# Optimization experiments

Measured on AMD Instinct MI355X. Metric: run time of the kernel, lower is better.

Reference implementation:

```python
import jax, jax.numpy as jnp
import numpy as np

NIBBLE_SHIFTS = jnp.arange(8, dtype=jnp.int32) * 4


def _unpack_int4(packed):
    # packed: [..., P] int32 -> [..., P*8] int32 values in [0, 15]
    vals = (packed[..., None] >> NIBBLE_SHIFTS) & 0xF
    return vals.reshape(*packed.shape[:-1], packed.shape[-1] * 8)


def setup_inputs() -> dict:
    key = jax.random.key(0)
    k1, k2, k3, k4, k5, k6 = jax.random.split(key, 6)
    M, K, N, G = 4096, 4096, 11008, 128
    inp = jax.random.normal(k1, (M, K), dtype=jnp.float32)
    qweight = jax.random.randint(k2, (K, N // 8), 0, 2147483647, dtype=jnp.int32)
    woq_scales = jax.random.uniform(k3, (K // G, N), dtype=jnp.float32)
    woq_qzeros = jax.random.randint(k4, (K // G, N // 8), 0, 2147483647, dtype=jnp.int32)
    woq_bias = jax.random.normal(k5, (N,), dtype=jnp.float32)
    mul = jax.random.normal(k6, (M, N), dtype=jnp.float32)
    return {"inp": inp, "qweight": qweight, "woq_scales": woq_scales,
            "woq_qzeros": woq_qzeros, "woq_bias": woq_bias, "mul": mul,
            "group_size": G}


def reference(inp, qweight, woq_scales, woq_qzeros, woq_bias, mul, group_size):
    K = qweight.shape[0]
    # dequantize int4 weights: w = (q - z) * scale, per group of `group_size` K-rows
    w_int = _unpack_int4(qweight).astype(jnp.float32)            # [K, N]
    z_int = _unpack_int4(woq_qzeros).astype(jnp.float32)         # [K/G, N]
    zeros_full = jnp.repeat(z_int, group_size, axis=0)           # [K, N]
    scales_full = jnp.repeat(woq_scales, group_size, axis=0)     # [K, N]
    w = (w_int - zeros_full) * scales_full                       # [K, N]
    woq_out = inp @ w + woq_bias                                 # [M, N]
    return jax.nn.silu(woq_out) * mul
```

## Files before the change

### kernel.cpp

```cpp
#include <hip/hip_runtime.h>
#include <hip/hip_bf16.h>

typedef __attribute__((ext_vector_type(8))) short short8;
typedef __attribute__((ext_vector_type(4))) short short4v;
typedef __attribute__((ext_vector_type(4))) float float4v;

__device__ __forceinline__ short f2bf(float f) {
  union { float f; unsigned u; } v; v.f = f;
  unsigned r = v.u + 0x7fffu + ((v.u >> 16) & 1u);
  return (short)(r >> 16);
}

typedef const __attribute__((address_space(1))) unsigned int* as1_u32p;
typedef __attribute__((address_space(3))) unsigned int* as3_u32p;

__device__ __forceinline__ void gl_lds16(const void* g, void* l) {
  __builtin_amdgcn_global_load_lds((as1_u32p)g, (as3_u32p)l, 16, 0, 0);
}

__global__ __launch_bounds__(256, 2)
void dequant_kernel(const int* __restrict__ qw,
                    const float* __restrict__ scales,
                    const int* __restrict__ qzeros,
                    short* __restrict__ Bt,
                    int K, int N, int G)
{
  __shared__ short Ls[128 * 64];
  const int N8  = N >> 3;
  const int k0  = blockIdx.x * 64;
  const int n80 = blockIdx.y * 16;
  const int g   = k0 / G;
  const int tid  = threadIdx.x;
  const int lane = tid & 63;
  const int w    = tid >> 6;

  const int4 q4 = *(const int4*)(qw + (size_t)(k0 + lane) * N8 + n80 + w * 4);
  const int4 z4 = *(const int4*)(qzeros + (size_t)g * N8 + n80 + w * 4);
  const int qa[4] = {q4.x, q4.y, q4.z, q4.w};
  const int za[4] = {z4.x, z4.y, z4.z, z4.w};

  #pragma unroll
  for (int it = 0; it < 4; ++it) {
    const int n8l = w * 4 + it;
    const float4v s0 = *(const float4v*)(scales + (size_t)g * N + (n80 + n8l) * 8);
    const float4v s1 = *(const float4v*)(scales + (size_t)g * N + (n80 + n8l) * 8 + 4);
    const float sc[8] = {s0[0], s0[1], s0[2], s0[3], s1[0], s1[1], s1[2], s1[3]};
    const int wq = qa[it], wz = za[it];
    #pragma unroll
    for (int j = 0; j < 8; ++j) {
      const float z = (float)((wz >> (4 * j)) & 0xF);
      const float q = (float)((wq >> (4 * j)) & 0xF);
      Ls[(n8l * 8 + j) * 64 + lane] = f2bf((q - z) * sc[j]);
    }
  }
  __syncthreads();

  #pragma unroll
  for (int it = 0; it < 4; ++it) {
    const int c   = tid + it * 256;
    const int row = c >> 3;
    const int off = (c & 7) * 8;
    const short8 v = *(const short8*)(&Ls[row * 64 + off]);
    *(short8*)(Bt + (size_t)(n80 * 8 + row) * K + k0 + off) = v;
  }
}

__global__ __launch_bounds__(256, 4)
void aconv_kernel(const float* __restrict__ in, short* __restrict__ out, long long n)
{
  const long long i = ((long long)blockIdx.x * blockDim.x + threadIdx.x) * 8;
  if (i >= n) return;
  const float4v a = *(const float4v*)(in + i);
  const float4v b = *(const float4v*)(in + i + 4);
  short8 h;
  h[0] = f2bf(a[0]); h[1] = f2bf(a[1]); h[2] = f2bf(a[2]); h[3] = f2bf(a[3]);
  h[4] = f2bf(b[0]); h[5] = f2bf(b[1]); h[6] = f2bf(b[2]); h[7] = f2bf(b[3]);
  *(short8*)(out + i) = h;
}

__global__ __launch_bounds__(512, 2)
void gemm256_silu_mul_kernel(const short* __restrict__ A,
                             const short* __restrict__ Bt,
                             const float* __restrict__ bias,
                             const float* __restrict__ mulp,
                             float*       __restrict__ out,
                             int M, int N, int K)
{
  __shared__ short L[2][2][16384];

  const int tid  = threadIdx.x;
  const int lane = tid & 63;
  const int wave = tid >> 6;
  const int wm   = wave >> 2;
  const int wn   = wave & 3;

  const int nwg = gridDim.x;
  const int q8 = nwg >> 3, r8 = nwg & 7;
  const int xcd = blockIdx.x & 7, sub = blockIdx.x >> 3;
  const int swz = (xcd < r8 ? xcd * (q8 + 1) : r8 * (q8 + 1) + (xcd - r8) * q8) + sub;
  const int nbx = N >> 8;
  const int bx = swz % nbx, by = swz / nbx;
  const int m0 = by << 8, n0 = bx << 8;

  const short* Ab = A  + (size_t)m0 * K;
  const short* Bb = Bt + (size_t)n0 * K;

  const int srow = lane >> 2;
  const int scol = (((lane & 3) ^ ((lane & 32) >> 4))) * 8;
  const int fm = lane & 15;
  const int ko = ((lane >> 4) * 8) ^ ((fm & 8) ? 16 : 0);

  const int BG0 = wave * 2;
  const int BG1 = wave * 2 + 1;
  const int AEg = (wave & 3) + (wave >> 2) * 8;
  const int ALg = AEg + 4;

  float4v acc[8][4];
  #pragma unroll
  for (int i = 0; i < 8; ++i)
    #pragma unroll
    for (int j = 0; j < 4; ++j)
      acc[i][j] = (float4v){0.f, 0.f, 0.f, 0.f};

  const int NT = K >> 6;

  auto stage2 = [&](int buf, int ab, int g, const short* __restrict__ base, int kk) {
    #pragma unroll
    for (int ks = 0; ks < 2; ++ks)
      gl_lds16(base + (size_t)(g * 16 + srow) * K + kk + ks * 32 + scol,
               &L[buf][ab][(g * 2 + ks) * 512]);
  };

  stage2(0, 1, BG0, Bb, 0);
  stage2(0, 1, BG1, Bb, 0);
  stage2(0, 0, AEg, Ab, 0);
  stage2(0, 0, ALg, Ab, 0);
  asm volatile("s_waitcnt vmcnt(2)" ::: "memory");
  __builtin_amdgcn_s_barrier();

  for (int t = 0; t < NT; ++t) {
    const int cur = t & 1;
    const int nxt = cur ^ 1;
    const int kk1 = (t + 1) << 6;
    const bool pf = (t + 1) < NT;

    short8 af[4][2], bf[4][2];

    #pragma unroll
    for (int i = 0; i < 4; ++i)
      #pragma unroll
      for (int ks = 0; ks < 2; ++ks)
        af[i][ks] = *(const short8*)(
            &L[cur][0][((wm * 8 + i) * 2 + ks) * 512 + fm * 32 + ko]);
    #pragma unroll
    for (int j = 0; j < 2; ++j)
      #pragma unroll
      for (int ks = 0; ks < 2; ++ks)
        bf[j][ks] = *(const short8*)(
            &L[cur][1][((wn * 4 + j) * 2 + ks) * 512 + fm * 32 + ko]);
    if (pf) stage2(nxt, 1, BG0, Bb, kk1);
    __builtin_amdgcn_s_barrier();
    asm volatile("s_waitcnt lgkmcnt(0)" ::: "memory");
    __builtin_amdgcn_sched_barrier(0);
    __builtin_amdgcn_s_setprio(1);
    #pragma unroll
    for (int i = 0; i < 4; ++i)
      #pragma unroll
      for (int j = 0; j < 2; ++j)
        #pragma unroll
        for (int ks = 0; ks < 2; ++ks)
          acc[i][j] = __builtin_amdgcn_mfma_f32_16x16x32_bf16(
              af[i][ks], bf[j][ks], acc[i][j], 0, 0, 0);
    __builtin_amdgcn_s_setprio(0);
    __builtin_amdgcn_s_barrier();

    #pragma unroll
    for (int j = 2; j < 4; ++j)
      #pragma unroll
      for (int ks = 0; ks < 2; ++ks)
        bf[j][ks] = *(const short8*)(
            &L[cur][1][((wn * 4 + j) * 2 + ks) * 512 + fm * 32 + ko]);
    if (pf) stage2(nxt, 1, BG1, Bb, kk1);
    __builtin_amdgcn_s_barrier();
    asm volatile("s_waitcnt lgkmcnt(0)" ::: "memory");
    __builtin_amdgcn_sched_barrier(0);
    __builtin_amdgcn_s_setprio(1);
    #pragma unroll
    for (int i = 0; i < 4; ++i)
      #pragma unroll
      for (int j = 2; j < 4; ++j)
        #pragma unroll
        for (int ks = 0; ks < 2; ++ks)
          acc[i][j] = __builtin_amdgcn_mfma_f32_16x16x32_bf16(
              af[i][ks], bf[j][ks], acc[i][j], 0, 0, 0);
    __builtin_amdgcn_s_setprio(0);
    if (pf) { asm volatile("s_waitcnt vmcnt(4)" ::: "memory"); }
    else    { asm volatile("s_waitcnt vmcnt(0)" ::: "memory"); }
    __builtin_amdgcn_s_barrier();

    #pragma unroll
    for (int i = 0; i < 4; ++i)
      #pragma unroll
      for (int ks = 0; ks < 2; ++ks)
        af[i][ks] = *(const short8*)(
            &L[cur][0][((wm * 8 + 4 + i) * 2 + ks) * 512 + fm * 32 + ko]);
    if (pf) stage2(nxt, 0, AEg, Ab, kk1);
    __builtin_amdgcn_s_barrier();
    asm volatile("s_waitcnt lgkmcnt(0)" ::: "memory");
    __builtin_amdgcn_sched_barrier(0);
    __builtin_amdgcn_s_setprio(1);
    #pragma unroll
    for (int i = 0; i < 4; ++i)
      #pragma unroll
      for (int j = 0; j < 2; ++j)
        #pragma unroll
        for (int ks = 0; ks < 2; ++ks)
          acc[4 + i][j] = __builtin_amdgcn_mfma_f32_16x16x32_bf16(
              af[i][ks], bf[j][ks], acc[4 + i][j], 0, 0, 0);
    __builtin_amdgcn_s_setprio(0);
    __builtin_amdgcn_s_barrier();

    if (pf) stage2(nxt, 0, ALg, Ab, kk1);
    __builtin_amdgcn_s_barrier();
    __builtin_amdgcn_s_setprio(1);
    #pragma unroll
    for (int i = 0; i < 4; ++i)
      #pragma unroll
      for (int j = 2; j < 4; ++j)
        #pragma unroll
        for (int ks = 0; ks < 2; ++ks)
          acc[4 + i][j] = __builtin_amdgcn_mfma_f32_16x16x32_bf16(
              af[i][ks], bf[j][ks], acc[4 + i][j], 0, 0, 0);
    __builtin_amdgcn_s_setprio(0);
    if (pf) { asm volatile("s_waitcnt vmcnt(2)" ::: "memory"); }
    __builtin_amdgcn_s_barrier();
  }

  const int cn  = lane & 15;
  const int cr4 = (lane >> 4) * 4;
  #pragma unroll
  for (int mt = 0; mt < 8; ++mt) {
    #pragma unroll
    for (int nt = 0; nt < 4; ++nt) {
      const int n  = n0 + wn * 64 + nt * 16 + cn;
      const float bn = bias[n];
      #pragma unroll
      for (int i = 0; i < 4; ++i) {
        const int m = m0 + wm * 128 + mt * 16 + cr4 + i;
        float x = acc[mt][nt][i] + bn;
        float s = x / (1.0f + __expf(-x));
        out[(size_t)m * N + n] = s * mulp[(size_t)m * N + n];
      }
    }
  }
}

__global__ __launch_bounds__(256, 2)
void gemm_silu_mul_kernel(const short* __restrict__ A,
                          const short* __restrict__ Bt,
                          const float* __restrict__ bias,
                          const float* __restrict__ mulp,
                          float*       __restrict__ out,
                          int M, int N, int K)
{
  __shared__ short As[128 * 64];
  __shared__ short Bs[128 * 64];

  const int tid  = threadIdx.x;
  const int lane = tid & 63;
  const int wave = tid >> 6;
  const int wr = (wave >> 1) * 64;
  const int wc = (wave & 1) * 64;
  const int m0 = blockIdx.y * 128;
  const int n0 = blockIdx.x * 128;

  float4v acc[4][4];
  #pragma unroll
  for (int i = 0; i < 4; ++i)
    #pragma unroll
    for (int j = 0; j < 4; ++j)
      acc[i][j] = (float4v){0.f, 0.f, 0.f, 0.f};

  const int fm = lane & 15;
  const int fk = (lane >> 4) * 8;
  const int srow = lane >> 3;
  const int scol = (lane & 7) * 8;

  for (int k0 = 0; k0 < K; k0 += 64) {
    #pragma unroll
    for (int c = 0; c < 4; ++c) {
      const int chunk = wave * 4 + c;
      const int row   = chunk * 8 + srow;
      gl_lds16(A  + (size_t)(m0 + row) * K + k0 + scol, &As[chunk * 512]);
      gl_lds16(Bt + (size_t)(n0 + row) * K + k0 + scol, &Bs[chunk * 512]);
    }
    __syncthreads();

    #pragma unroll
    for (int ks = 0; ks < 64; ks += 32) {
      short8 a[4], b[4];
      #pragma unroll
      for (int mt = 0; mt < 4; ++mt)
        a[mt] = *(const short8*)(&As[(wr + mt * 16 + fm) * 64 + ks + fk]);
      #pragma unroll
      for (int nt = 0; nt < 4; ++nt)
        b[nt] = *(const short8*)(&Bs[(wc + nt * 16 + fm) * 64 + ks + fk]);
      #pragma unroll
      for (int mt = 0; mt < 4; ++mt)
        #pragma unroll
        for (int nt = 0; nt < 4; ++nt)
          acc[mt][nt] = __builtin_amdgcn_mfma_f32_16x16x32_bf16(a[mt], b[nt], acc[mt][nt], 0, 0, 0);
    }
    __syncthreads();
  }

  const int cn = lane & 15;
  const int cr = (lane >> 4) * 4;
  #pragma unroll
  for (int mt = 0; mt < 4; ++mt) {
    #pragma unroll
    for (int nt = 0; nt < 4; ++nt) {
      const int n  = n0 + wc + nt * 16 + cn;
      const float bn = bias[n];
      #pragma unroll
      for (int i = 0; i < 4; ++i) {
        const int m = m0 + wr + mt * 16 + cr + i;
        float x = acc[mt][nt][i] + bn;
        float s = x / (1.0f + __expf(-x));
        out[(size_t)m * N + n] = s * mulp[(size_t)m * N + n];
      }
    }
  }
}

#define BM 128
#define BN 128
#define BK 64
#define LDA 72
#define LDB 72

__global__ __launch_bounds__(256, 2)
void woq_silu_mul_kernel(const float* __restrict__ inp, const int* __restrict__ qw,
                         const float* __restrict__ scales, const int* __restrict__ qzeros,
                         const float* __restrict__ bias, const float* __restrict__ mulp,
                         float* __restrict__ out, int M, int N, int K, int G)
{
  __shared__ short As[BM * LDA];
  __shared__ short Bs[BN * LDB];
  const int tid  = threadIdx.x;
  const int lane = tid & 63;
  const int wave = tid >> 6;
  const int wr = (wave >> 1) * 64;
  const int wc = (wave & 1) * 64;
  const int m0 = blockIdx.y * BM;
  const int n0 = blockIdx.x * BN;
  const int N8 = N >> 3;
  float4v acc[4][4];
  #pragma unroll
  for (int i = 0; i < 4; ++i)
    #pragma unroll
    for (int j = 0; j < 4; ++j)
      acc[i][j] = (float4v){0.f, 0.f, 0.f, 0.f};
  const int n8l  = tid >> 4;
  const int kloc = (tid & 15) * 4;
  const int fm = lane & 15;
  const int fk = (lane >> 4) * 8;
  for (int k0 = 0; k0 < K; k0 += BK) {
    #pragma unroll
    for (int i = 0; i < 8; ++i) {
      int f = tid + i * 256;
      int row = f >> 4;
      int col = (f & 15) * 4;
      float4v a4 = *(const float4v*)(inp + (size_t)(m0 + row) * K + k0 + col);
      short4v h;
      h[0] = f2bf(a4[0]); h[1] = f2bf(a4[1]); h[2] = f2bf(a4[2]); h[3] = f2bf(a4[3]);
      *(short4v*)(&As[row * LDA + col]) = h;
    }
    {
      const int g = k0 / G;
      const int n8g = (n0 >> 3) + n8l;
      const int zw = qzeros[(size_t)g * N8 + n8g];
      const float4v s0 = *(const float4v*)(scales + (size_t)g * N + n0 + n8l * 8);
      const float4v s1 = *(const float4v*)(scales + (size_t)g * N + n0 + n8l * 8 + 4);
      float sc[8] = {s0[0], s0[1], s0[2], s0[3], s1[0], s1[1], s1[2], s1[3]};
      int w[4];
      #pragma unroll
      for (int kk = 0; kk < 4; ++kk)
        w[kk] = qw[(size_t)(k0 + kloc + kk) * N8 + n8g];
      #pragma unroll
      for (int j = 0; j < 8; ++j) {
        const float zj = (float)((zw >> (4 * j)) & 0xF);
        const float sj = sc[j];
        short4v h;
        #pragma unroll
        for (int kk = 0; kk < 4; ++kk) {
          int q = (w[kk] >> (4 * j)) & 0xF;
          h[kk] = f2bf(((float)q - zj) * sj);
        }
        *(short4v*)(&Bs[(n8l * 8 + j) * LDB + kloc]) = h;
      }
    }
    __syncthreads();
    #pragma unroll
    for (int ks = 0; ks < BK; ks += 32) {
      short8 a[4], b[4];
      #pragma unroll
      for (int mt = 0; mt < 4; ++mt)
        a[mt] = *(const short8*)(&As[(wr + mt * 16 + fm) * LDA + ks + fk]);
      #pragma unroll
      for (int nt = 0; nt < 4; ++nt)
        b[nt] = *(const short8*)(&Bs[(wc + nt * 16 + fm) * LDB + ks + fk]);
      #pragma unroll
      for (int mt = 0; mt < 4; ++mt)
        #pragma unroll
        for (int nt = 0; nt < 4; ++nt)
          acc[mt][nt] = __builtin_amdgcn_mfma_f32_16x16x32_bf16(a[mt], b[nt], acc[mt][nt], 0, 0, 0);
    }
    __syncthreads();
  }
  const int cn = lane & 15;
  const int cr = (lane >> 4) * 4;
  #pragma unroll
  for (int mt = 0; mt < 4; ++mt) {
    #pragma unroll
    for (int nt = 0; nt < 4; ++nt) {
      const int n = n0 + wc + nt * 16 + cn;
      const float bn = bias[n];
      #pragma unroll
      for (int i = 0; i < 4; ++i) {
        const int m = m0 + wr + mt * 16 + cr + i;
        float x = acc[mt][nt][i] + bn;
        float s = x / (1.0f + __expf(-x));
        out[(size_t)m * N + n] = s * mulp[(size_t)m * N + n];
      }
    }
  }
}

extern "C" void kernel_launch(void* const* d_in, const int* in_sizes, int n_in,
                              void* d_out, int out_size, void* d_ws, size_t ws_size,
                              hipStream_t stream) {
  const float* inp    = (const float*)d_in[0];
  const int*   qw     = (const int*)d_in[1];
  const float* scales = (const float*)d_in[2];
  const int*   qzeros = (const int*)d_in[3];
  const float* bias   = (const float*)d_in[4];
  const float* mulp   = (const float*)d_in[5];
  float*       out    = (float*)d_out;

  const int N = in_sizes[4];
  const int K = (int)(((long long)in_sizes[1] * 8) / N);
  const int M = (int)((long long)in_sizes[0] / K);
  const int G = K / (in_sizes[2] / N);

  const size_t btBytes = (size_t)N * K * sizeof(short);
  const size_t aBytes  = (size_t)M * K * sizeof(short);

  if (ws_size >= btBytes + aBytes) {
    short* Bt  = (short*)d_ws;
    short* Abf = (short*)((char*)d_ws + btBytes);

    dim3 dq_grid(K / 64, (N / 8) / 16);
    dequant_kernel<<<dq_grid, dim3(256), 0, stream>>>(qw, scales, qzeros, Bt, K, N, G);

    const long long nA = (long long)M * K;
    aconv_kernel<<<dim3((unsigned)((nA / 8 + 255) / 256)), dim3(256), 0, stream>>>(inp, Abf, nA);

    if ((M & 255) == 0 && (N & 255) == 0 && (K & 63) == 0) {
      dim3 grid((unsigned)((N >> 8) * (M >> 8)));
      gemm256_silu_mul_kernel<<<grid, dim3(512), 0, stream>>>(Abf, Bt, bias, mulp, out, M, N, K);
    } else {
      dim3 grid(N / 128, M / 128);
      gemm_silu_mul_kernel<<<grid, dim3(256), 0, stream>>>(Abf, Bt, bias, mulp, out, M, N, K);
    }
  } else {
    dim3 grid(N / BN, M / BM);
    woq_silu_mul_kernel<<<grid, dim3(256), 0, stream>>>(inp, qw, scales, qzeros,
                                                        bias, mulp, out, M, N, K, G);
  }
}
```

Before: 699.9 us.

## Rewrite dequant kernel with wider N tiles and reorder GEMM B/A prefetch stages

Replaces the dequantize kernel with a variant in which each block covers 256 N columns by 64 K rows. Scales are loaded into registers once per thread, and tiles are transposed through a padded LDS buffer so Bt is written with 16-byte stores. The old kernel is kept as a fallback for shapes where N is not a multiple of 256. The GEMM main loop also reorders its prefetches: the A tile is issued first and the B tiles are split into even/odd column halves, with the vmcnt waits adjusted to match. This aims to overlap global loads with MFMA work better, but wrong waitcnt values could cause stale LDS reads.

```diff
diff --git a/kernel.cpp b/kernel.cpp
--- a/kernel.cpp
+++ b/kernel.cpp
@@ -18,12 +18,65 @@
   __builtin_amdgcn_global_load_lds((as1_u32p)g, (as3_u32p)l, 16, 0, 0);
 }
 
-__global__ __launch_bounds__(256, 2)
+__global__ __launch_bounds__(256, 4)
 void dequant_kernel(const int* __restrict__ qw,
                     const float* __restrict__ scales,
                     const int* __restrict__ qzeros,
                     short* __restrict__ Bt,
                     int K, int N, int G)
+{
+  constexpr int KP = 72;
+  __shared__ short Ls[256 * KP];
+  const int N8  = N >> 3;
+  const int k0  = blockIdx.x * 64;
+  const int n0  = blockIdx.y * 256;
+  const int n80 = blockIdx.y * 32;
+  const int g   = k0 / G;
+  const int t   = threadIdx.x;
+  const int kloc = t >> 3;
+  const int w4   = (t & 7) * 4;
+
+  const int4 z4 = *(const int4*)(qzeros + (size_t)g * N8 + n80 + w4);
+  const int za[4] = {z4.x, z4.y, z4.z, z4.w};
+  float sc[32];
+  #pragma unroll
+  for (int ii = 0; ii < 8; ++ii)
+    *(float4v*)(sc + ii * 4) =
+        *(const float4v*)(scales + (size_t)g * N + n0 + w4 * 8 + ii * 4);
+
+  #pragma unroll
+  for (int kh = 0; kh < 2; ++kh) {
+    const int k = kloc + kh * 32;
+    const int4 q4 = *(const int4*)(qw + (size_t)(k0 + k) * N8 + n80 + w4);
+    const int qa[4] = {q4.x, q4.y, q4.z, q4.w};
+    #pragma unroll
+    for (int ii = 0; ii < 4; ++ii) {
+      #pragma unroll
+      for (int j = 0; j < 8; ++j) {
+        const float z = (float)((za[ii] >> (4 * j)) & 0xF);
+        const float q = (float)((qa[ii] >> (4 * j)) & 0xF);
+        Ls[(w4 * 8 + ii * 8 + j) * KP + k] = f2bf((q - z) * sc[ii * 8 + j]);
+      }
+    }
+  }
+  __syncthreads();
+
+  #pragma unroll
+  for (int it = 0; it < 8; ++it) {
+    const int idx = t + it * 256;
+    const int row = idx >> 3;
+    const int ch  = (idx & 7) * 8;
+    const short8 v = *(const short8*)(&Ls[row * KP + ch]);
+    *(short8*)(Bt + (size_t)(n0 + row) * K + k0 + ch) = v;
+  }
+}
+
+__global__ __launch_bounds__(256, 2)
+void dequant_kernel_v0(const int* __restrict__ qw,
+                       const float* __restrict__ scales,
+                       const int* __restrict__ qzeros,
+                       short* __restrict__ Bt,
+                       int K, int N, int G)
 {
   __shared__ short Ls[128 * 64];
   const int N8  = N >> 3;
@@ -131,11 +184,11 @@
                &L[buf][ab][(g * 2 + ks) * 512]);
   };
 
+  stage2(0, 0, AEg, Ab, 0);
   stage2(0, 1, BG0, Bb, 0);
   stage2(0, 1, BG1, Bb, 0);
-  stage2(0, 0, AEg, Ab, 0);
   stage2(0, 0, ALg, Ab, 0);
-  asm volatile("s_waitcnt vmcnt(2)" ::: "memory");
+  asm volatile("s_waitcnt vmcnt(4)" ::: "memory");
   __builtin_amdgcn_s_barrier();
 
   for (int t = 0; t < NT; ++t) {
@@ -153,7 +206,31 @@
         af[i][ks] = *(const short8*)(
             &L[cur][0][((wm * 8 + i) * 2 + ks) * 512 + fm * 32 + ko]);
     #pragma unroll
-    for (int j = 0; j < 2; ++j)
+    for (int j = 0; j < 4; j += 2)
+      #pragma unroll
+      for (int ks = 0; ks < 2; ++ks)
+        bf[j][ks] = *(const short8*)(
+            &L[cur][1][((wn * 4 + j) * 2 + ks) * 512 + fm * 32 + ko]);
+    if (pf) stage2(nxt, 0, AEg, Ab, kk1);
+    __builtin_amdgcn_s_barrier();
+    asm volatile("s_waitcnt lgkmcnt(0)" ::: "memory");
+    __builtin_amdgcn_sched_barrier(0);
+    __builtin_amdgcn_s_setprio(1);
+    #pragma unroll
+    for (int i = 0; i < 4; ++i)
+      #pragma unroll
+      for (int j = 0; j < 4; j += 2)
+        #pragma unroll
+        for (int ks = 0; ks < 2; ++ks)
+          acc[i][j] = __builtin_amdgcn_mfma_f32_16x16x32_bf16(
+              af[i][ks], bf[j][ks], acc[i][j], 0, 0, 0);
+    __builtin_amdgcn_s_setprio(0);
+    if (pf) { asm volatile("s_waitcnt vmcnt(4)" ::: "memory"); }
+    else    { asm volatile("s_waitcnt vmcnt(2)" ::: "memory"); }
+    __builtin_amdgcn_s_barrier();
+
+    #pragma unroll
+    for (int j = 1; j < 4; j += 2)
       #pragma unroll
       for (int ks = 0; ks < 2; ++ks)
         bf[j][ks] = *(const short8*)(
@@ -166,29 +243,7 @@
     #pragma unroll
     for (int i = 0; i < 4; ++i)
       #pragma unroll
-      for (int j = 0; j < 2; ++j)
-        #pragma unroll
-        for (int ks = 0; ks < 2; ++ks)
-          acc[i][j] = __builtin_amdgcn_mfma_f32_16x16x32_bf16(
-              af[i][ks], bf[j][ks], acc[i][j], 0, 0, 0);
-    __builtin_amdgcn_s_setprio(0);
-    __builtin_amdgcn_s_barrier();
-
-    #pragma unroll
-    for (int j = 2; j < 4; ++j)
-      #pragma unroll
-      for (int ks = 0; ks < 2; ++ks)
-        bf[j][ks] = *(const short8*)(
-            &L[cur][1][((wn * 4 + j) * 2 + ks) * 512 + fm * 32 + ko]);
-    if (pf) stage2(nxt, 1, BG1, Bb, kk1);
-    __builtin_amdgcn_s_barrier();
-    asm volatile("s_waitcnt lgkmcnt(0)" ::: "memory");
-    __builtin_amdgcn_sched_barrier(0);
-    __builtin_amdgcn_s_setprio(1);
-    #pragma unroll
-    for (int i = 0; i < 4; ++i)
-      #pragma unroll
-      for (int j = 2; j < 4; ++j)
+      for (int j = 1; j < 4; j += 2)
         #pragma unroll
         for (int ks = 0; ks < 2; ++ks)
           acc[i][j] = __builtin_amdgcn_mfma_f32_16x16x32_bf16(
@@ -204,7 +259,7 @@
       for (int ks = 0; ks < 2; ++ks)
         af[i][ks] = *(const short8*)(
             &L[cur][0][((wm * 8 + 4 + i) * 2 + ks) * 512 + fm * 32 + ko]);
-    if (pf) stage2(nxt, 0, AEg, Ab, kk1);
+    if (pf) stage2(nxt, 1, BG1, Bb, kk1);
     __builtin_amdgcn_s_barrier();
     asm volatile("s_waitcnt lgkmcnt(0)" ::: "memory");
     __builtin_amdgcn_sched_barrier(0);
@@ -212,7 +267,7 @@
     #pragma unroll
     for (int i = 0; i < 4; ++i)
       #pragma unroll
-      for (int j = 0; j < 2; ++j)
+      for (int j = 0; j < 4; j += 2)
         #pragma unroll
         for (int ks = 0; ks < 2; ++ks)
           acc[4 + i][j] = __builtin_amdgcn_mfma_f32_16x16x32_bf16(
@@ -226,13 +281,13 @@
     #pragma unroll
     for (int i = 0; i < 4; ++i)
       #pragma unroll
-      for (int j = 2; j < 4; ++j)
+      for (int j = 1; j < 4; j += 2)
         #pragma unroll
         for (int ks = 0; ks < 2; ++ks)
           acc[4 + i][j] = __builtin_amdgcn_mfma_f32_16x16x32_bf16(
               af[i][ks], bf[j][ks], acc[4 + i][j], 0, 0, 0);
     __builtin_amdgcn_s_setprio(0);
-    if (pf) { asm volatile("s_waitcnt vmcnt(2)" ::: "memory"); }
+    if (pf) { asm volatile("s_waitcnt vmcnt(4)" ::: "memory"); }
     __builtin_amdgcn_s_barrier();
   }
 
@@ -460,8 +515,13 @@
     short* Bt  = (short*)d_ws;
     short* Abf = (short*)((char*)d_ws + btBytes);
 
-    dim3 dq_grid(K / 64, (N / 8) / 16);
-    dequant_kernel<<<dq_grid, dim3(256), 0, stream>>>(qw, scales, qzeros, Bt, K, N, G);
+    if ((N & 255) == 0 && (K & 63) == 0 && (64 % (K / (in_sizes[2] / N) > 64 ? 64 : 1)) == 0) {
+      dim3 dq_grid(K / 64, N / 256);
+      dequant_kernel<<<dq_grid, dim3(256), 0, stream>>>(qw, scales, qzeros, Bt, K, N, G);
+    } else {
+      dim3 dq_grid(K / 64, (N / 8) / 16);
+      dequant_kernel_v0<<<dq_grid, dim3(256), 0, stream>>>(qw, scales, qzeros, Bt, K, N, G);
+    }
 
     const long long nA = (long long)M * K;
     aconv_kernel<<<dim3((unsigned)((nA / 8 + 255) / 256)), dim3(256), 0, stream>>>(inp, Abf, nA);
```

Measured after the change: 707.5 us. No clear change (+1.1%).
